# Performance work log

Measured on AMD Instinct MI355X. Metric: run time of the kernel, lower is better.

Reference implementation:

```python
import jax, jax.numpy as jnp
import numpy as np

N_QUBITS = 4
N_LAYERS = 6
BATCH = 131072

# Pauli-Z expectation sign table: qubit q corresponds to bit (N_QUBITS-1-q) of the
# flattened state index (axis q+1 of the [B,2,2,2,2] state is most-significant first).
_idx = np.arange(2 ** N_QUBITS)
Z_SIGNS = jnp.asarray(1.0 - 2.0 * ((_idx[:, None] >> (N_QUBITS - 1 - np.arange(N_QUBITS))) & 1), dtype=jnp.float32)  # [16, 4]


def _apply_1q(state, U, q):
    # state: [B, 2,2,2,2]; U: [2,2] (shared) or [B,2,2] (per-sample)
    s = jnp.moveaxis(state, q + 1, -1)
    if U.ndim == 3:
        s = jnp.einsum('bij,b...j->b...i', U, s)
    else:
        s = jnp.einsum('ij,b...j->b...i', U, s)
    return jnp.moveaxis(s, -1, q + 1)


def _apply_cnot(state, c, t):
    # flip target axis on the control=1 slice
    s = jnp.moveaxis(state, (c + 1, t + 1), (-2, -1))
    s = jnp.concatenate([s[..., :1, :], s[..., 1:, ::-1]], axis=-2)
    return jnp.moveaxis(s, (-2, -1), (c + 1, t + 1))


def _rot(phi, theta, omega):
    # PennyLane Rot(phi, theta, omega) = RZ(omega) @ RY(theta) @ RZ(phi)
    ct = jnp.cos(theta / 2)
    st = jnp.sin(theta / 2)
    ep = jnp.exp(-0.5j * (phi + omega))  # e^{-i(phi+omega)/2}
    em = jnp.exp(0.5j * (phi - omega))   # e^{ i(phi-omega)/2}
    row0 = jnp.stack([ep * ct, -em * st])
    row1 = jnp.stack([jnp.conj(em) * st, jnp.conj(ep) * ct])
    return jnp.stack([row0, row1]).astype(jnp.complex64)


def _forward(inputs, rotations):
    B = inputs.shape[0]
    # |0...0> batched state
    state = jnp.zeros((B,) + (2,) * N_QUBITS, dtype=jnp.complex64)
    state = state.at[(slice(None),) + (0,) * N_QUBITS].set(1.0)

    # AngleEmbedding: RX(x_q) on wire q (per-sample gates)
    c = jnp.cos(inputs / 2)
    s = jnp.sin(inputs / 2)
    for q in range(N_QUBITS):
        U = jnp.stack([
            jnp.stack([c[:, q] + 0j, -1j * s[:, q]], axis=-1),
            jnp.stack([-1j * s[:, q], c[:, q] + 0j], axis=-1),
        ], axis=-2).astype(jnp.complex64)  # [B,2,2]
        state = _apply_1q(state, U, q)

    # StronglyEntanglingLayers
    for l in range(N_LAYERS):
        for q in range(N_QUBITS):
            state = _apply_1q(state, _rot(rotations[l, q, 0], rotations[l, q, 1], rotations[l, q, 2]), q)
        r = l % (N_QUBITS - 1) + 1  # default imprimitive range pattern
        for q in range(N_QUBITS):
            state = _apply_cnot(state, q, (q + r) % N_QUBITS)

    probs = (state.real ** 2 + state.imag ** 2).reshape(B, 2 ** N_QUBITS)  # [B,16]
    return (probs @ Z_SIGNS).astype(jnp.float32)  # [B, N_QUBITS] = <Z_q>


def setup_inputs() -> dict:
    key = jax.random.key(0)
    k1, k2 = jax.random.split(key)
    inputs = jax.random.normal(k1, (BATCH, N_QUBITS), dtype=jnp.float32)
    # keras 'random_uniform' initializer: U(-0.05, 0.05)
    rotations = jax.random.uniform(k2, (N_LAYERS, N_QUBITS, 3), dtype=jnp.float32, minval=-0.05, maxval=0.05)
    return {"inputs": inputs, "rotations": rotations}


def reference(inputs, rotations):
    return _forward(inputs, rotations)
```

## Files before the change

kernel.cpp:

```cpp
#include <hip/hip_runtime.h>
#include <math.h>

#define NQ 4
#define NL 6
#define DIM 16
#define BLOCK 256

__global__ __launch_bounds__(BLOCK) void vqc_kernel(
    const float* __restrict__ inputs,
    const float* __restrict__ rot,
    float* __restrict__ out,
    int batch)
{
    __shared__ float U[NL * NQ][8];

    const int tid = threadIdx.x;
    if (tid < NL * NQ) {
        float phi = rot[tid * 3 + 0];
        float theta = rot[tid * 3 + 1];
        float omega = rot[tid * 3 + 2];
        float st, ct;
        __sincosf(0.5f * theta, &st, &ct);
        float a = 0.5f * (phi + omega);
        float b = 0.5f * (phi - omega);
        float sa, ca, sb, cb;
        __sincosf(a, &sa, &ca);
        __sincosf(b, &sb, &cb);
        U[tid][0] = ca * ct;
        U[tid][1] = -sa * ct;
        U[tid][2] = -cb * st;
        U[tid][3] = -sb * st;
        U[tid][4] = cb * st;
        U[tid][5] = -sb * st;
        U[tid][6] = ca * ct;
        U[tid][7] = sa * ct;
    }
    __syncthreads();

    const int b = blockIdx.x * BLOCK + tid;
    if (b >= batch) return;

    const float4 x = ((const float4*)inputs)[b];
    float c[NQ], s[NQ];
    __sincosf(0.5f * x.x, &s[0], &c[0]);
    __sincosf(0.5f * x.y, &s[1], &c[1]);
    __sincosf(0.5f * x.z, &s[2], &c[2]);
    __sincosf(0.5f * x.w, &s[3], &c[3]);

    float sr[DIM], si[DIM];
#pragma unroll
    for (int i = 0; i < DIM; ++i) {
        float mag = (((i >> 3) & 1) ? s[0] : c[0])
                  * (((i >> 2) & 1) ? s[1] : c[1])
                  * (((i >> 1) & 1) ? s[2] : c[2])
                  * (((i >> 0) & 1) ? s[3] : c[3]);
        const int k = (((i >> 3) & 1) + ((i >> 2) & 1) + ((i >> 1) & 1) + (i & 1)) & 3;
        sr[i] = (k == 0) ? mag : ((k == 2) ? -mag : 0.0f);
        si[i] = (k == 1) ? -mag : ((k == 3) ? mag : 0.0f);
    }

#pragma unroll 1
    for (int half = 0; half < 2; ++half) {
        const int ubase = half * (3 * NQ);
#pragma unroll
        for (int li = 0; li < 3; ++li) {
#pragma unroll
            for (int q = 0; q < NQ; ++q) {
                const float* u = U[ubase + li * NQ + q];
                const float u00r = u[0], u00i = u[1], u01r = u[2], u01i = u[3];
                const float u10r = u[4], u10i = u[5], u11r = u[6], u11i = u[7];
                const int m = 1 << (3 - q);
#pragma unroll
                for (int i = 0; i < DIM; ++i) {
                    if (!(i & m)) {
                        const int j = i | m;
                        const float a0r = sr[i], a0i = si[i];
                        const float a1r = sr[j], a1i = si[j];
                        sr[i] = u00r * a0r - u00i * a0i + u01r * a1r - u01i * a1i;
                        si[i] = u00r * a0i + u00i * a0r + u01r * a1i + u01i * a1r;
                        sr[j] = u10r * a0r - u10i * a0i + u11r * a1r - u11i * a1i;
                        si[j] = u10r * a0i + u10i * a0r + u11r * a1i + u11i * a1r;
                    }
                }
            }
            const int r = li + 1;
#pragma unroll
            for (int q = 0; q < NQ; ++q) {
                const int t = (q + r) & 3;
                const int cm = 1 << (3 - q);
                const int tm = 1 << (3 - t);
#pragma unroll
                for (int i = 0; i < DIM; ++i) {
                    if ((i & cm) && !(i & tm)) {
                        const int j = i | tm;
                        float tr = sr[i]; sr[i] = sr[j]; sr[j] = tr;
                        float ti = si[i]; si[i] = si[j]; si[j] = ti;
                    }
                }
            }
        }
    }

    float e0 = 0.f, e1 = 0.f, e2 = 0.f, e3 = 0.f;
#pragma unroll
    for (int i = 0; i < DIM; ++i) {
        const float p = sr[i] * sr[i] + si[i] * si[i];
        e0 += ((i >> 3) & 1) ? -p : p;
        e1 += ((i >> 2) & 1) ? -p : p;
        e2 += ((i >> 1) & 1) ? -p : p;
        e3 += ((i >> 0) & 1) ? -p : p;
    }
    ((float4*)out)[b] = make_float4(e0, e1, e2, e3);
}

extern "C" void kernel_launch(void* const* d_in, const int* in_sizes, int n_in,
                              void* d_out, int out_size, void* d_ws, size_t ws_size,
                              hipStream_t stream) {
    const float* inputs = (const float*)d_in[0];
    const float* rot = (const float*)d_in[1];
    float* out = (float*)d_out;
    const int batch = in_sizes[0] / NQ;
    const int grid = (batch + BLOCK - 1) / BLOCK;
    vqc_kernel<<<grid, BLOCK, 0, stream>>>(inputs, rot, out, batch);
}
```

Measured before the change: 69.60 us.

## Split each sample's state vector across two lanes with packed float2 math

Each batch sample is now handled by a pair of threads, each holding half of the 16-amplitude state as float2 vectors. Gates on qubit 0 exchange data between the pair with cross-lane shuffles, and qubit 3 uses in-register vector swizzles. CNOT layers are rewritten as permutations that mix lane selects and shuffles. This doubles thread count to raise parallelism and lower register pressure, and uses packed FP32 ops. The cost is extra shuffle traffic, redundant sincos per pair, and twice the launched threads.

```diff
diff --git a/kernel.cpp b/kernel.cpp
--- a/kernel.cpp
+++ b/kernel.cpp
@@ -3,8 +3,9 @@
 
 #define NQ 4
 #define NL 6
-#define DIM 16
 #define BLOCK 256
+
+typedef float v2 __attribute__((ext_vector_type(2)));
 
 __global__ __launch_bounds__(BLOCK) void vqc_kernel(
     const float* __restrict__ inputs,
@@ -37,7 +38,9 @@
     }
     __syncthreads();
 
-    const int b = blockIdx.x * BLOCK + tid;
+    const int gid = blockIdx.x * BLOCK + tid;
+    const int b = gid >> 1;
+    const int p = gid & 1;
     if (b >= batch) return;
 
     const float4 x = ((const float4*)inputs)[b];
@@ -47,16 +50,25 @@
     __sincosf(0.5f * x.z, &s[2], &c[2]);
     __sincosf(0.5f * x.w, &s[3], &c[3]);
 
-    float sr[DIM], si[DIM];
-#pragma unroll
-    for (int i = 0; i < DIM; ++i) {
-        float mag = (((i >> 3) & 1) ? s[0] : c[0])
-                  * (((i >> 2) & 1) ? s[1] : c[1])
-                  * (((i >> 1) & 1) ? s[2] : c[2])
-                  * (((i >> 0) & 1) ? s[3] : c[3]);
-        const int k = (((i >> 3) & 1) + ((i >> 2) & 1) + ((i >> 1) & 1) + (i & 1)) & 3;
-        sr[i] = (k == 0) ? mag : ((k == 2) ? -mag : 0.0f);
-        si[i] = (k == 1) ? -mag : ((k == 3) ? mag : 0.0f);
+    v2 sr[4], si[4];
+    {
+        const float f0 = p ? s[0] : c[0];
+#pragma unroll
+        for (int k = 0; k < 4; ++k) {
+#pragma unroll
+            for (int slot = 0; slot < 2; ++slot) {
+                const float mag = f0 * (((k >> 1) & 1) ? s[1] : c[1])
+                                     * ((k & 1) ? s[2] : c[2])
+                                     * (slot ? s[3] : c[3]);
+                const int n = ((k >> 1) & 1) + (k & 1) + slot;
+                const float xr_ = (n == 0) ? mag : ((n == 2) ? -mag : 0.f);
+                const float xi_ = (n == 1) ? -mag : ((n == 3) ? mag : 0.f);
+                const float rr = p ? xi_ : xr_;
+                const float ri = p ? -xr_ : xi_;
+                if (slot == 0) { sr[k].x = rr; si[k].x = ri; }
+                else           { sr[k].y = rr; si[k].y = ri; }
+            }
+        }
     }
 
 #pragma unroll 1
@@ -64,53 +76,136 @@
         const int ubase = half * (3 * NQ);
 #pragma unroll
         for (int li = 0; li < 3; ++li) {
-#pragma unroll
-            for (int q = 0; q < NQ; ++q) {
+            {
+                const float* u = U[ubase + li * NQ + 0];
+                const float ar = p ? u[6] : u[0], ai = p ? u[7] : u[1];
+                const float br = p ? u[4] : u[2], bi = p ? u[5] : u[3];
+#pragma unroll
+                for (int k = 0; k < 4; ++k) {
+                    const v2 xr = sr[k], xi = si[k];
+                    v2 yr, yi;
+                    yr.x = __shfl_xor(xr.x, 1); yr.y = __shfl_xor(xr.y, 1);
+                    yi.x = __shfl_xor(xi.x, 1); yi.y = __shfl_xor(xi.y, 1);
+                    sr[k] = ar * xr - ai * xi + br * yr - bi * yi;
+                    si[k] = ar * xi + ai * xr + br * yi + bi * yr;
+                }
+            }
+#pragma unroll
+            for (int q = 1; q <= 2; ++q) {
                 const float* u = U[ubase + li * NQ + q];
                 const float u00r = u[0], u00i = u[1], u01r = u[2], u01i = u[3];
                 const float u10r = u[4], u10i = u[5], u11r = u[6], u11i = u[7];
-                const int m = 1 << (3 - q);
-#pragma unroll
-                for (int i = 0; i < DIM; ++i) {
-                    if (!(i & m)) {
-                        const int j = i | m;
-                        const float a0r = sr[i], a0i = si[i];
-                        const float a1r = sr[j], a1i = si[j];
-                        sr[i] = u00r * a0r - u00i * a0i + u01r * a1r - u01i * a1i;
-                        si[i] = u00r * a0i + u00i * a0r + u01r * a1i + u01i * a1r;
-                        sr[j] = u10r * a0r - u10i * a0i + u11r * a1r - u11i * a1i;
-                        si[j] = u10r * a0i + u10i * a0r + u11r * a1i + u11i * a1r;
+                const int m = (q == 1) ? 2 : 1;
+#pragma unroll
+                for (int k = 0; k < 4; ++k) {
+                    if (!(k & m)) {
+                        const int k2 = k | m;
+                        const v2 a0r = sr[k], a0i = si[k];
+                        const v2 a1r = sr[k2], a1i = si[k2];
+                        sr[k]  = u00r * a0r - u00i * a0i + u01r * a1r - u01i * a1i;
+                        si[k]  = u00r * a0i + u00i * a0r + u01r * a1i + u01i * a1r;
+                        sr[k2] = u10r * a0r - u10i * a0i + u11r * a1r - u11i * a1i;
+                        si[k2] = u10r * a0i + u10i * a0r + u11r * a1i + u11i * a1r;
                     }
                 }
             }
-            const int r = li + 1;
-#pragma unroll
-            for (int q = 0; q < NQ; ++q) {
-                const int t = (q + r) & 3;
-                const int cm = 1 << (3 - q);
-                const int tm = 1 << (3 - t);
-#pragma unroll
-                for (int i = 0; i < DIM; ++i) {
-                    if ((i & cm) && !(i & tm)) {
-                        const int j = i | tm;
-                        float tr = sr[i]; sr[i] = sr[j]; sr[j] = tr;
-                        float ti = si[i]; si[i] = si[j]; si[j] = ti;
-                    }
+            {
+                const float* u = U[ubase + li * NQ + 3];
+                const v2 dr = {u[0], u[6]}, di = {u[1], u[7]};
+                const v2 er = {u[2], u[4]}, ei = {u[3], u[5]};
+#pragma unroll
+                for (int k = 0; k < 4; ++k) {
+                    const v2 xr = sr[k], xi = si[k];
+                    const v2 yr = __builtin_shufflevector(xr, xr, 1, 0);
+                    const v2 yi = __builtin_shufflevector(xi, xi, 1, 0);
+                    sr[k] = dr * xr - di * xi + er * yr - ei * yi;
+                    si[k] = dr * xi + di * xr + er * yi + ei * yr;
+                }
+            }
+            if (li == 0) {
+                { v2 a=sr[0],b_=sr[2]; sr[0]=p?b_:a; sr[2]=p?a:b_;
+                  v2 ai_=si[0],bi_=si[2]; si[0]=p?bi_:ai_; si[2]=p?ai_:bi_;
+                  v2 c_=sr[1],d_=sr[3]; sr[1]=p?d_:c_; sr[3]=p?c_:d_;
+                  v2 ci_=si[1],di_=si[3]; si[1]=p?di_:ci_; si[3]=p?ci_:di_; }
+                { v2 t=sr[2]; sr[2]=sr[3]; sr[3]=t; t=si[2]; si[2]=si[3]; si[3]=t; }
+                sr[1]=__builtin_shufflevector(sr[1],sr[1],1,0);
+                si[1]=__builtin_shufflevector(si[1],si[1],1,0);
+                sr[3]=__builtin_shufflevector(sr[3],sr[3],1,0);
+                si[3]=__builtin_shufflevector(si[3],si[3],1,0);
+#pragma unroll
+                for (int k = 0; k < 4; ++k) {
+                    sr[k].y = __shfl_xor(sr[k].y, 1);
+                    si[k].y = __shfl_xor(si[k].y, 1);
+                }
+            } else if (li == 1) {
+                { v2 a=sr[0],b_=sr[1]; sr[0]=p?b_:a; sr[1]=p?a:b_;
+                  v2 ai_=si[0],bi_=si[1]; si[0]=p?bi_:ai_; si[1]=p?ai_:bi_;
+                  v2 c_=sr[2],d_=sr[3]; sr[2]=p?d_:c_; sr[3]=p?c_:d_;
+                  v2 ci_=si[2],di_=si[3]; si[2]=p?di_:ci_; si[3]=p?ci_:di_; }
+                sr[2]=__builtin_shufflevector(sr[2],sr[2],1,0);
+                si[2]=__builtin_shufflevector(si[2],si[2],1,0);
+                sr[3]=__builtin_shufflevector(sr[3],sr[3],1,0);
+                si[3]=__builtin_shufflevector(si[3],si[3],1,0);
+#pragma unroll
+                for (int k = 1; k < 4; k += 2) {
+                    sr[k].x = __shfl_xor(sr[k].x, 1); sr[k].y = __shfl_xor(sr[k].y, 1);
+                    si[k].x = __shfl_xor(si[k].x, 1); si[k].y = __shfl_xor(si[k].y, 1);
+                }
+#pragma unroll
+                for (int k = 0; k < 2; ++k) {
+                    const int k2 = k | 2;
+                    v2 Ar=sr[k], Br=sr[k2], Ai=si[k], Bi=si[k2];
+                    sr[k]=__builtin_shufflevector(Ar,Br,0,3);
+                    sr[k2]=__builtin_shufflevector(Br,Ar,0,3);
+                    si[k]=__builtin_shufflevector(Ai,Bi,0,3);
+                    si[k2]=__builtin_shufflevector(Bi,Ai,0,3);
+                }
+            } else {
+#pragma unroll
+                for (int k = 0; k < 4; ++k) {
+                    const v2 wr=__builtin_shufflevector(sr[k],sr[k],1,0);
+                    const v2 wi=__builtin_shufflevector(si[k],si[k],1,0);
+                    sr[k] = p ? wr : sr[k];
+                    si[k] = p ? wi : si[k];
+                }
+#pragma unroll
+                for (int k = 2; k < 4; ++k) {
+                    sr[k].x = __shfl_xor(sr[k].x, 1); sr[k].y = __shfl_xor(sr[k].y, 1);
+                    si[k].x = __shfl_xor(si[k].x, 1); si[k].y = __shfl_xor(si[k].y, 1);
+                }
+                { v2 t=sr[1]; sr[1]=sr[3]; sr[3]=t; t=si[1]; si[1]=si[3]; si[3]=t; }
+#pragma unroll
+                for (int k = 0; k < 4; k += 2) {
+                    const int k2 = k | 1;
+                    v2 Ar=sr[k], Br=sr[k2], Ai=si[k], Bi=si[k2];
+                    sr[k]=__builtin_shufflevector(Ar,Br,0,3);
+                    sr[k2]=__builtin_shufflevector(Br,Ar,0,3);
+                    si[k]=__builtin_shufflevector(Ai,Bi,0,3);
+                    si[k2]=__builtin_shufflevector(Bi,Ai,0,3);
                 }
             }
         }
     }
 
-    float e0 = 0.f, e1 = 0.f, e2 = 0.f, e3 = 0.f;
-#pragma unroll
-    for (int i = 0; i < DIM; ++i) {
-        const float p = sr[i] * sr[i] + si[i] * si[i];
-        e0 += ((i >> 3) & 1) ? -p : p;
-        e1 += ((i >> 2) & 1) ? -p : p;
-        e2 += ((i >> 1) & 1) ? -p : p;
-        e3 += ((i >> 0) & 1) ? -p : p;
-    }
-    ((float4*)out)[b] = make_float4(e0, e1, e2, e3);
+    v2 a0 = {0.f,0.f}, a1 = {0.f,0.f}, a2 = {0.f,0.f}, a3 = {0.f,0.f};
+    const v2 sgn3 = {1.f, -1.f};
+#pragma unroll
+    for (int k = 0; k < 4; ++k) {
+        const v2 pk = sr[k]*sr[k] + si[k]*si[k];
+        a0 += pk;
+        a1 += ((k >> 1) & 1) ? -pk : pk;
+        a2 += (k & 1) ? -pk : pk;
+        a3 += pk * sgn3;
+    }
+    float e0 = a0.x + a0.y; e0 = p ? -e0 : e0;
+    float e1 = a1.x + a1.y;
+    float e2 = a2.x + a2.y;
+    float e3 = a3.x + a3.y;
+    e0 += __shfl_xor(e0, 1);
+    e1 += __shfl_xor(e1, 1);
+    e2 += __shfl_xor(e2, 1);
+    e3 += __shfl_xor(e3, 1);
+    if (p == 0) ((float4*)out)[b] = make_float4(e0, e1, e2, e3);
 }
 
 extern "C" void kernel_launch(void* const* d_in, const int* in_sizes, int n_in,
@@ -120,6 +215,7 @@
     const float* rot = (const float*)d_in[1];
     float* out = (float*)d_out;
     const int batch = in_sizes[0] / NQ;
-    const int grid = (batch + BLOCK - 1) / BLOCK;
+    const long long threads = 2LL * batch;
+    const int grid = (int)((threads + BLOCK - 1) / BLOCK);
     vqc_kernel<<<grid, BLOCK, 0, stream>>>(inputs, rot, out, batch);
 }
```

Result: faster. 65.70 us (-5.6%).

## Precompute fused 16x16 circuit unitary per block and apply as matvec

Applied to the files above, without the earlier changes.

Every block now builds the full 16x16 unitary of the entangling layers by having 16 threads each propagate one basis vector, and stores it in shared memory as packed float2 columns. Each sample then applies this matrix to its product-state embedding vector, using the i^k phase structure to avoid complex multiplies and packed float2 arithmetic. This replaces roughly 24 per-sample gate applications with a single 16x16 complex matvec. The cost is redundant unitary construction in every block, with 16 threads doing serial work while the rest wait at a barrier, plus many shared-memory reads per sample.

```diff
diff --git a/kernel.cpp b/kernel.cpp
--- a/kernel.cpp
+++ b/kernel.cpp
@@ -6,6 +6,8 @@
 #define DIM 16
 #define BLOCK 256
 
+typedef float v2 __attribute__((ext_vector_type(2)));
+
 __global__ __launch_bounds__(BLOCK) void vqc_kernel(
     const float* __restrict__ inputs,
     const float* __restrict__ rot,
@@ -13,6 +15,8 @@
     int batch)
 {
     __shared__ float U[NL * NQ][8];
+    __shared__ v2 WR[DIM][8];
+    __shared__ v2 WI[DIM][8];
 
     const int tid = threadIdx.x;
     if (tid < NL * NQ) {
@@ -37,80 +41,101 @@
     }
     __syncthreads();
 
+    if (tid < DIM) {
+        float ar[DIM], ai[DIM];
+#pragma unroll
+        for (int i = 0; i < DIM; ++i) { ar[i] = (i == tid) ? 1.f : 0.f; ai[i] = 0.f; }
+#pragma unroll 1
+        for (int half = 0; half < 2; ++half) {
+            const int ubase = half * (3 * NQ);
+#pragma unroll
+            for (int li = 0; li < 3; ++li) {
+#pragma unroll
+                for (int q = 0; q < NQ; ++q) {
+                    const float* u = U[ubase + li * NQ + q];
+                    const float u00r = u[0], u00i = u[1], u01r = u[2], u01i = u[3];
+                    const float u10r = u[4], u10i = u[5], u11r = u[6], u11i = u[7];
+                    const int m = 1 << (3 - q);
+#pragma unroll
+                    for (int i = 0; i < DIM; ++i) {
+                        if (!(i & m)) {
+                            const int j = i | m;
+                            const float a0r = ar[i], a0i = ai[i];
+                            const float a1r = ar[j], a1i = ai[j];
+                            ar[i] = u00r * a0r - u00i * a0i + u01r * a1r - u01i * a1i;
+                            ai[i] = u00r * a0i + u00i * a0r + u01r * a1i + u01i * a1r;
+                            ar[j] = u10r * a0r - u10i * a0i + u11r * a1r - u11i * a1i;
+                            ai[j] = u10r * a0i + u10i * a0r + u11r * a1i + u11i * a1r;
+                        }
+                    }
+                }
+                const int r = li + 1;
+#pragma unroll
+                for (int q = 0; q < NQ; ++q) {
+                    const int t = (q + r) & 3;
+                    const int cm = 1 << (3 - q);
+                    const int tm = 1 << (3 - t);
+#pragma unroll
+                    for (int i = 0; i < DIM; ++i) {
+                        if ((i & cm) && !(i & tm)) {
+                            const int j = i | tm;
+                            float tr = ar[i]; ar[i] = ar[j]; ar[j] = tr;
+                            float ti = ai[i]; ai[i] = ai[j]; ai[j] = ti;
+                        }
+                    }
+                }
+            }
+        }
+#pragma unroll
+        for (int rp = 0; rp < 8; ++rp) {
+            WR[tid][rp] = (v2){ar[2 * rp], ar[2 * rp + 1]};
+            WI[tid][rp] = (v2){ai[2 * rp], ai[2 * rp + 1]};
+        }
+    }
+    __syncthreads();
+
     const int b = blockIdx.x * BLOCK + tid;
     if (b >= batch) return;
 
     const float4 x = ((const float4*)inputs)[b];
-    float c[NQ], s[NQ];
-    __sincosf(0.5f * x.x, &s[0], &c[0]);
-    __sincosf(0.5f * x.y, &s[1], &c[1]);
-    __sincosf(0.5f * x.z, &s[2], &c[2]);
-    __sincosf(0.5f * x.w, &s[3], &c[3]);
+    float cc[NQ], ss[NQ];
+    __sincosf(0.5f * x.x, &ss[0], &cc[0]);
+    __sincosf(0.5f * x.y, &ss[1], &cc[1]);
+    __sincosf(0.5f * x.z, &ss[2], &cc[2]);
+    __sincosf(0.5f * x.w, &ss[3], &cc[3]);
 
-    float sr[DIM], si[DIM];
+    v2 yr[8], yi[8];
 #pragma unroll
-    for (int i = 0; i < DIM; ++i) {
-        float mag = (((i >> 3) & 1) ? s[0] : c[0])
-                  * (((i >> 2) & 1) ? s[1] : c[1])
-                  * (((i >> 1) & 1) ? s[2] : c[2])
-                  * (((i >> 0) & 1) ? s[3] : c[3]);
-        const int k = (((i >> 3) & 1) + ((i >> 2) & 1) + ((i >> 1) & 1) + (i & 1)) & 3;
-        sr[i] = (k == 0) ? mag : ((k == 2) ? -mag : 0.0f);
-        si[i] = (k == 1) ? -mag : ((k == 3) ? mag : 0.0f);
-    }
-
-#pragma unroll 1
-    for (int half = 0; half < 2; ++half) {
-        const int ubase = half * (3 * NQ);
+    for (int rp = 0; rp < 8; ++rp) { yr[rp] = (v2){0.f, 0.f}; yi[rp] = (v2){0.f, 0.f}; }
 #pragma unroll
-        for (int li = 0; li < 3; ++li) {
+    for (int cI = 0; cI < DIM; ++cI) {
+        const float m = (((cI >> 3) & 1) ? ss[0] : cc[0])
+                      * (((cI >> 2) & 1) ? ss[1] : cc[1])
+                      * (((cI >> 1) & 1) ? ss[2] : cc[2])
+                      * (((cI >> 0) & 1) ? ss[3] : cc[3]);
+        const int k = (((cI >> 3) & 1) + ((cI >> 2) & 1) + ((cI >> 1) & 1) + (cI & 1)) & 3;
 #pragma unroll
-            for (int q = 0; q < NQ; ++q) {
-                const float* u = U[ubase + li * NQ + q];
-                const float u00r = u[0], u00i = u[1], u01r = u[2], u01i = u[3];
-                const float u10r = u[4], u10i = u[5], u11r = u[6], u11i = u[7];
-                const int m = 1 << (3 - q);
-#pragma unroll
-                for (int i = 0; i < DIM; ++i) {
-                    if (!(i & m)) {
-                        const int j = i | m;
-                        const float a0r = sr[i], a0i = si[i];
-                        const float a1r = sr[j], a1i = si[j];
-                        sr[i] = u00r * a0r - u00i * a0i + u01r * a1r - u01i * a1i;
-                        si[i] = u00r * a0i + u00i * a0r + u01r * a1i + u01i * a1r;
-                        sr[j] = u10r * a0r - u10i * a0i + u11r * a1r - u11i * a1i;
-                        si[j] = u10r * a0i + u10i * a0r + u11r * a1i + u11i * a1r;
-                    }
-                }
-            }
-            const int r = li + 1;
-#pragma unroll
-            for (int q = 0; q < NQ; ++q) {
-                const int t = (q + r) & 3;
-                const int cm = 1 << (3 - q);
-                const int tm = 1 << (3 - t);
-#pragma unroll
-                for (int i = 0; i < DIM; ++i) {
-                    if ((i & cm) && !(i & tm)) {
-                        const int j = i | tm;
-                        float tr = sr[i]; sr[i] = sr[j]; sr[j] = tr;
-                        float ti = si[i]; si[i] = si[j]; si[j] = ti;
-                    }
-                }
-            }
+        for (int rp = 0; rp < 8; ++rp) {
+            const v2 wr = WR[cI][rp], wi = WI[cI][rp];
+            if (k == 0)      { yr[rp] += wr * m; yi[rp] += wi * m; }
+            else if (k == 1) { yr[rp] += wi * m; yi[rp] -= wr * m; }
+            else if (k == 2) { yr[rp] -= wr * m; yi[rp] -= wi * m; }
+            else             { yr[rp] -= wi * m; yi[rp] += wr * m; }
         }
     }
 
-    float e0 = 0.f, e1 = 0.f, e2 = 0.f, e3 = 0.f;
+    v2 a0 = {0.f, 0.f}, a1 = {0.f, 0.f}, a2 = {0.f, 0.f}, a3 = {0.f, 0.f};
+    const v2 sgn3 = {1.f, -1.f};
 #pragma unroll
-    for (int i = 0; i < DIM; ++i) {
-        const float p = sr[i] * sr[i] + si[i] * si[i];
-        e0 += ((i >> 3) & 1) ? -p : p;
-        e1 += ((i >> 2) & 1) ? -p : p;
-        e2 += ((i >> 1) & 1) ? -p : p;
-        e3 += ((i >> 0) & 1) ? -p : p;
+    for (int rp = 0; rp < 8; ++rp) {
+        const v2 p2 = yr[rp] * yr[rp] + yi[rp] * yi[rp];
+        a0 += ((rp >> 2) & 1) ? -p2 : p2;
+        a1 += ((rp >> 1) & 1) ? -p2 : p2;
+        a2 += (rp & 1) ? -p2 : p2;
+        a3 += p2 * sgn3;
     }
-    ((float4*)out)[b] = make_float4(e0, e1, e2, e3);
+    ((float4*)out)[b] = make_float4(a0.x + a0.y, a1.x + a1.y,
+                                    a2.x + a2.y, a3.x + a3.y);
 }
 
 extern "C" void kernel_launch(void* const* d_in, const int* in_sizes, int n_in,
```

New measurement: 69.31 us. No clear change (-0.4%).
